# Optimization experiments

Measured on AMD Instinct MI355X. Metric: run time of the kernel, lower is better.

The kernel has to match this reference:

```python
import jax, jax.numpy as jnp
import numpy as np

N = 100000
EPS = 1e-5
NEG_SLOPE = 0.2


def gat_conv(x, src, dst, W, a_src, a_dst, b):
    # x: [N, din]; W: [dout, din]; a_src/a_dst/b: [dout]
    h = x @ W.T                              # [N, dout]
    alpha_s = h @ a_src                      # [N]
    alpha_d = h @ a_dst                      # [N]
    e = jax.nn.leaky_relu(alpha_s[src] + alpha_d[dst], NEG_SLOPE)  # [E]
    # segment softmax over incoming edges of each destination node
    emax = jax.ops.segment_max(e, dst, num_segments=N)
    ex = jnp.exp(e - emax[dst])
    denom = jax.ops.segment_sum(ex, dst, num_segments=N)
    alpha = ex / denom[dst]                  # [E]
    out = jax.ops.segment_sum(alpha[:, None] * h[src], dst, num_segments=N)
    return out + b


def batch_norm(x, gamma, beta):
    mu = jnp.mean(x, axis=0)
    var = jnp.var(x, axis=0)
    return gamma * (x - mu) * jax.lax.rsqrt(var + EPS) + beta


def setup_inputs() -> dict:
    key = jax.random.key(0)
    ks = jax.random.split(key, 20)
    din, dh, dout = 128, 128, 128
    E = 1600000
    x = jax.random.normal(ks[0], (N, din), dtype=jnp.float32)
    edge_index = jax.random.randint(ks[1], (2, E), 0, N, dtype=jnp.int32)
    def glorot(k, shape):
        fan = sum(shape)
        s = jnp.sqrt(6.0 / fan)
        return jax.random.uniform(k, shape, dtype=jnp.float32, minval=-s, maxval=s)
    inp = {"x": x, "edge_index": edge_index}
    dims = [(din, dh), (dh, dh), (dh, dout)]
    for l, (di, do) in enumerate(dims):
        inp[f"W{l}"] = glorot(ks[2 + 4 * l], (do, di))
        inp[f"a_src{l}"] = glorot(ks[3 + 4 * l], (do,)) * 0.1
        inp[f"a_dst{l}"] = glorot(ks[4 + 4 * l], (do,)) * 0.1
        inp[f"b{l}"] = jnp.zeros((do,), dtype=jnp.float32)
    for l in range(2):
        inp[f"gamma{l}"] = jnp.ones((dh,), dtype=jnp.float32)
        inp[f"beta{l}"] = jnp.zeros((dh,), dtype=jnp.float32)
    return inp


def reference(x, edge_index, W0, a_src0, a_dst0, b0, W1, a_src1, a_dst1, b1,
              W2, a_src2, a_dst2, b2, gamma0, beta0, gamma1, beta1):
    # add self-loops (PyG GATConv default)
    ar = jnp.arange(N, dtype=edge_index.dtype)
    src = jnp.concatenate([edge_index[0], ar])
    dst = jnp.concatenate([edge_index[1], ar])
    h = gat_conv(x, src, dst, W0, a_src0, a_dst0, b0)
    h = jax.nn.relu(batch_norm(h, gamma0, beta0))
    h = gat_conv(h, src, dst, W1, a_src1, a_dst1, b1)
    h = jax.nn.relu(batch_norm(h, gamma1, beta1))
    out = gat_conv(h, src, dst, W2, a_src2, a_dst2, b2)
    return out
```

## Files before the change

kernel.cpp:

```cpp
#include <hip/hip_runtime.h>
#include <cstdint>
#include <cstddef>

#define NN 100000
#define NP 100096
#define EE 1600000
#define ET 1700000
#define NBKT 196
#define TILE 2048
#define STAT_BLOCKS 400

typedef short  bf16x8 __attribute__((ext_vector_type(8)));
typedef float  f32x4  __attribute__((ext_vector_type(4)));

__device__ __forceinline__ unsigned short f2bf(float f) {
    unsigned int x = __builtin_bit_cast(unsigned int, f);
    x += 0x7FFFu + ((x >> 16) & 1u);
    return (unsigned short)(x >> 16);
}
__device__ __forceinline__ unsigned int pk2(float lo, float hi) {
    return ((unsigned int)f2bf(hi) << 16) | (unsigned int)f2bf(lo);
}
__device__ __forceinline__ float bflo(unsigned int u) {
    return __builtin_bit_cast(float, u << 16);
}
__device__ __forceinline__ float bfhi(unsigned int u) {
    return __builtin_bit_cast(float, u & 0xFFFF0000u);
}
__device__ __forceinline__ int unperm(int j) { return ((j & 7) << 4) | (j >> 3); }

__global__ void k_pre(const int* __restrict__ ei,
                      const float* __restrict__ W0, const float* __restrict__ W1,
                      const float* __restrict__ W2, unsigned short* __restrict__ Wb,
                      int* __restrict__ btot)
{
    const int t = threadIdx.x;
    const int b = blockIdx.x;
    if (b < 256) {
        __shared__ int h[256];
        h[t] = 0;
        __syncthreads();
        for (int e = b * 256 + t; e < ET; e += 256 * 256) {
            int d = (e < EE) ? ei[EE + e] : (e - EE);
            atomicAdd(&h[d >> 9], 1);
        }
        __syncthreads();
        if (h[t]) atomicAdd(&btot[t], h[t]);
    } else {
        int i = (b - 256) * 256 + t;
        int layer = i >> 14;
        const float* W = (layer == 0) ? W0 : (layer == 1) ? W1 : W2;
        int o  = i & 16383;
        int f  = o >> 3, e = o & 7;
        int nt = f >> 8, k0 = (f >> 6) & 3, lane = f & 63;
        int c  = lane & 15, q = lane >> 4;
        int k  = k0 * 32 + q * 8 + e;
        int col = (layer == 0) ? k : unperm(k);
        Wb[i] = f2bf(W[(nt * 16 + c) * 128 + col]);
    }
}

__global__ void k_bscan(const int* __restrict__ btot, int* __restrict__ bstart,
                        int* __restrict__ bcur, int* __restrict__ off) {
    __shared__ int s[256];
    int t = threadIdx.x;
    int v = (t < NBKT) ? btot[t] : 0;
    s[t] = v;
    __syncthreads();
    for (int o = 1; o < 256; o <<= 1) {
        int a = (t >= o) ? s[t - o] : 0;
        __syncthreads();
        s[t] += a;
        __syncthreads();
    }
    int ex = s[t] - v;
    if (t <= NBKT) bstart[t] = (t < NBKT) ? ex : ET;
    if (t == NBKT - 1) bstart[NBKT] = s[t];
    bcur[t] = ex;
    if (t == 0) off[NN] = ET;
}

__global__ __launch_bounds__(256) void k_bucket(
    const int* __restrict__ ei, int* __restrict__ bcur, unsigned int* __restrict__ bucketed)
{
    __shared__ int h4[4][256], woff[4][256], loff[256], gbase[256], sc[256];
    __shared__ unsigned int stage[TILE];
    __shared__ int gaddr[TILE];
    __shared__ int stot_s;
    const int t = threadIdx.x;
    const int w = t >> 6;
    const int e0 = blockIdx.x * TILE;

    h4[0][t] = 0; h4[1][t] = 0; h4[2][t] = 0; h4[3][t] = 0;
    __syncthreads();

    unsigned int pk[TILE / 256];
    int bk[TILE / 256];
#pragma unroll
    for (int i = 0; i < TILE / 256; ++i) {
        int e = e0 + i * 256 + t;
        bk[i] = -1;
        if (e < ET) {
            int s, d;
            if (e < EE) { s = ei[e]; d = ei[EE + e]; } else { s = e - EE; d = s; }
            bk[i] = d >> 9;
            pk[i] = ((unsigned int)(d & 511) << 17) | (unsigned int)s;
            atomicAdd(&h4[w][bk[i]], 1);
        }
    }
    __syncthreads();

    int h0 = h4[0][t], h1 = h4[1][t], h2 = h4[2][t], h3 = h4[3][t];
    int tot = h0 + h1 + h2 + h3;
    sc[t] = tot;
    __syncthreads();
    for (int o = 1; o < 256; o <<= 1) {
        int a = (t >= o) ? sc[t - o] : 0;
        __syncthreads();
        sc[t] += a;
        __syncthreads();
    }
    int lo = sc[t] - tot;
    loff[t] = lo;
    woff[0][t] = lo;
    woff[1][t] = lo + h0;
    woff[2][t] = lo + h0 + h1;
    woff[3][t] = lo + h0 + h1 + h2;
    if (t < NBKT && tot) gbase[t] = atomicAdd(&bcur[t], tot);
    if (t == 255) stot_s = sc[255];
    h4[0][t] = 0; h4[1][t] = 0; h4[2][t] = 0; h4[3][t] = 0;
    __syncthreads();

#pragma unroll
    for (int i = 0; i < TILE / 256; ++i) {
        if (bk[i] >= 0) {
            int b = bk[i];
            int r = woff[w][b] + atomicAdd(&h4[w][b], 1);
            stage[r] = pk[i];
            gaddr[r] = gbase[b] + (r - loff[b]);
        }
    }
    __syncthreads();

    const int stot = stot_s;
    for (int j = t; j < stot; j += 256)
        bucketed[gaddr[j]] = stage[j];
}

__global__ __launch_bounds__(256) void k_csr(
    const unsigned int* __restrict__ bucketed, const int* __restrict__ bstart,
    int* __restrict__ off, int* __restrict__ srcs)
{
    __shared__ int h[512], sc2[512], c2[512], sp[256];
    const int t = threadIdx.x;
    const int b = blockIdx.x;
    const int beg = bstart[b], end = bstart[b + 1];
    const int cnt = end - beg;

    h[t] = 0; h[t + 256] = 0; c2[t] = 0; c2[t + 256] = 0;
    __syncthreads();
    for (int i = t; i < cnt; i += 256)
        atomicAdd(&h[bucketed[beg + i] >> 17], 1);
    __syncthreads();

    int a0 = h[2 * t], a1 = h[2 * t + 1];
    sp[t] = a0 + a1;
    __syncthreads();
    for (int o = 1; o < 256; o <<= 1) {
        int a = (t >= o) ? sp[t - o] : 0;
        __syncthreads();
        sp[t] += a;
        __syncthreads();
    }
    int ep = sp[t] - (a0 + a1);
    sc2[2 * t] = ep;
    sc2[2 * t + 1] = ep + a0;
    __syncthreads();

    const int d0 = b << 9;
#pragma unroll
    for (int k = t; k < 512; k += 256) {
        int d = d0 + k;
        if (d < NN) off[d] = beg + sc2[k];
    }

    for (int i = t; i < cnt; i += 256) {
        unsigned int v = bucketed[beg + i];
        int ld = v >> 17;
        int r = atomicAdd(&c2[ld], 1);
        srcs[beg + sc2[ld] + r] = (int)(v & 0x1FFFFu);
    }
}

template<int MODE>
__global__ __launch_bounds__(256) void k_mfma(
    const void* __restrict__ Xv, const unsigned short* __restrict__ Wb,
    const float* __restrict__ gsum, const float* __restrict__ gsq,
    const float* __restrict__ gamma, const float* __restrict__ beta,
    const float* __restrict__ asrc, const float* __restrict__ adst,
    unsigned short* __restrict__ Hb, float* __restrict__ AS, float* __restrict__ AD)
{
    __shared__ float scale_s[128], shift_s[128];
    const int t    = threadIdx.x;
    const int lane = t & 63;
    const int c    = lane & 15;
    const int q    = lane >> 4;
    const int r0   = blockIdx.x * 64 + (t >> 6) * 16;
    const int row  = r0 + c;

    if (MODE) {
        if (t < 128) {
            int ot = unperm(t);
            float mu  = gsum[t] * (1.f / NN);
            float var = gsq[t] * (1.f / NN) - mu * mu;
            float sc  = gamma[ot] * rsqrtf(var + 1e-5f);
            scale_s[t] = sc;
            shift_s[t] = beta[ot] - mu * sc;
        }
        __syncthreads();
    }

    union { uint4 u; bf16x8 v; } Af[4];
    if (row < NN) {
        if (MODE) {
            const unsigned short* xp = (const unsigned short*)Xv + ((size_t)row << 7) + (q << 3);
#pragma unroll
            for (int k0 = 0; k0 < 4; ++k0) {
                uint4 r = *(const uint4*)(xp + (k0 << 5));
                const int kb = (k0 << 5) + (q << 3);
                float a0 = bflo(r.x), a1 = bfhi(r.x), a2 = bflo(r.y), a3 = bfhi(r.y);
                float a4 = bflo(r.z), a5 = bfhi(r.z), a6 = bflo(r.w), a7 = bfhi(r.w);
                float4 sA = *(const float4*)&scale_s[kb];
                float4 sB = *(const float4*)&scale_s[kb + 4];
                float4 hA = *(const float4*)&shift_s[kb];
                float4 hB = *(const float4*)&shift_s[kb + 4];
                a0 = fmaxf(0.f, fmaf(a0, sA.x, hA.x));
                a1 = fmaxf(0.f, fmaf(a1, sA.y, hA.y));
                a2 = fmaxf(0.f, fmaf(a2, sA.z, hA.z));
                a3 = fmaxf(0.f, fmaf(a3, sA.w, hA.w));
                a4 = fmaxf(0.f, fmaf(a4, sB.x, hB.x));
                a5 = fmaxf(0.f, fmaf(a5, sB.y, hB.y));
                a6 = fmaxf(0.f, fmaf(a6, sB.z, hB.z));
                a7 = fmaxf(0.f, fmaf(a7, sB.w, hB.w));
                Af[k0].u.x = pk2(a0, a1);
                Af[k0].u.y = pk2(a2, a3);
                Af[k0].u.z = pk2(a4, a5);
                Af[k0].u.w = pk2(a6, a7);
            }
        } else {
            const float* xp = (const float*)Xv + ((size_t)row << 7) + (q << 3);
#pragma unroll
            for (int k0 = 0; k0 < 4; ++k0) {
                float4 a = *(const float4*)(xp + (k0 << 5));
                float4 b = *(const float4*)(xp + (k0 << 5) + 4);
                Af[k0].u.x = pk2(a.x, a.y);
                Af[k0].u.y = pk2(a.z, a.w);
                Af[k0].u.z = pk2(b.x, b.y);
                Af[k0].u.w = pk2(b.z, b.w);
            }
        }
    } else {
#pragma unroll
        for (int k0 = 0; k0 < 4; ++k0) Af[k0].u = make_uint4(0, 0, 0, 0);
    }

    f32x4 acc[8];
#pragma unroll
    for (int nt = 0; nt < 8; ++nt) acc[nt] = (f32x4){0.f, 0.f, 0.f, 0.f};

#pragma unroll
    for (int nt = 0; nt < 8; ++nt) {
        union { uint4 u; bf16x8 v; } Bf[4];
#pragma unroll
        for (int k0 = 0; k0 < 4; ++k0)
            Bf[k0].u = *(const uint4*)(Wb + ((size_t)(((nt << 2) + k0) * 64 + lane) << 3));
#pragma unroll
        for (int k0 = 0; k0 < 4; ++k0)
            acc[nt] = __builtin_amdgcn_mfma_f32_16x16x32_bf16(Af[k0].v, Bf[k0].v, acc[nt], 0, 0, 0);
    }

    float ps[4] = {0.f, 0.f, 0.f, 0.f}, pd[4] = {0.f, 0.f, 0.f, 0.f};
#pragma unroll
    for (int nt = 0; nt < 8; ++nt) {
        float av = asrc[nt * 16 + c];
        float dv = adst[nt * 16 + c];
#pragma unroll
        for (int r = 0; r < 4; ++r) {
            ps[r] = fmaf(acc[nt][r], av, ps[r]);
            pd[r] = fmaf(acc[nt][r], dv, pd[r]);
        }
    }
#pragma unroll
    for (int m = 1; m < 16; m <<= 1) {
#pragma unroll
        for (int r = 0; r < 4; ++r) { ps[r] += __shfl_xor(ps[r], m); pd[r] += __shfl_xor(pd[r], m); }
    }
    if (c == 0) {
#pragma unroll
        for (int r = 0; r < 4; ++r) {
            int grow = r0 + q * 4 + r;
            if (grow < NN) { AS[grow] = ps[r]; AD[grow] = pd[r]; }
        }
    }

#pragma unroll
    for (int r = 0; r < 4; ++r) {
        int grow = r0 + q * 4 + r;
        if (grow < NN) {
            uint4 o;
            o.x = pk2(acc[0][r], acc[1][r]);
            o.y = pk2(acc[2][r], acc[3][r]);
            o.z = pk2(acc[4][r], acc[5][r]);
            o.w = pk2(acc[6][r], acc[7][r]);
            *(uint4*)(Hb + ((size_t)grow << 7) + (c << 3)) = o;
        }
    }
}

template<int OUTBF>
__global__ __launch_bounds__(256) void k_agg(
    const int* __restrict__ off, const int* __restrict__ srcs,
    const unsigned short* __restrict__ Hb, const float* __restrict__ AS,
    const float* __restrict__ AD, const float* __restrict__ bias,
    void* __restrict__ OUT)
{
    __shared__ uint2 s_e[4][64];
    const int wid  = threadIdx.x >> 6;
    const int lane = threadIdx.x & 63;
    const int g    = lane >> 4;
    const int x16  = lane & 15;
    const int n    = blockIdx.x * 4 + wid;
    const int beg = off[n], end = off[n + 1];
    const float adn = AD[n];

    float acc[8];
#pragma unroll
    for (int i = 0; i < 8; ++i) acc[i] = 0.f;
    float den = 0.f;

    for (int base = beg; base < end; base += 64) {
        int cnt = end - base; if (cnt > 64) cnt = 64;
        float wgt = 0.f; int s = 0;
        if (lane < cnt) {
            s = srcs[base + lane];
            float e = AS[s] + adn;
            e = (e > 0.f) ? e : 0.2f * e;
            wgt = __expf(e);
        }
        s_e[wid][lane] = make_uint2((unsigned int)s, __builtin_bit_cast(unsigned int, wgt));
        den += wgt;
        int rounds = (cnt + 3) >> 2;
        for (int j = 0; j < rounds; ++j) {
            uint2 ew = s_e[wid][(j << 2) + g];
            float wq = __builtin_bit_cast(float, ew.y);
            uint4 u = *((const uint4*)(Hb + ((size_t)ew.x << 7)) + x16);
            acc[0] = fmaf(wq, bflo(u.x), acc[0]);
            acc[1] = fmaf(wq, bfhi(u.x), acc[1]);
            acc[2] = fmaf(wq, bflo(u.y), acc[2]);
            acc[3] = fmaf(wq, bfhi(u.y), acc[3]);
            acc[4] = fmaf(wq, bflo(u.z), acc[4]);
            acc[5] = fmaf(wq, bfhi(u.z), acc[5]);
            acc[6] = fmaf(wq, bflo(u.w), acc[6]);
            acc[7] = fmaf(wq, bfhi(u.w), acc[7]);
        }
    }

#pragma unroll
    for (int i = 0; i < 8; ++i) {
        acc[i] += __shfl_xor(acc[i], 16);
        acc[i] += __shfl_xor(acc[i], 32);
    }
#pragma unroll
    for (int o = 32; o; o >>= 1) den += __shfl_xor(den, o);
    float inv = 1.f / den;

    if (g == 0) {
        float o8[8];
#pragma unroll
        for (int i = 0; i < 8; ++i)
            o8[i] = fmaf(acc[i], inv, bias[i * 16 + x16]);
        if (OUTBF) {
            uint4 pkd;
            pkd.x = pk2(o8[0], o8[1]); pkd.y = pk2(o8[2], o8[3]);
            pkd.z = pk2(o8[4], o8[5]); pkd.w = pk2(o8[6], o8[7]);
            *(uint4*)((unsigned short*)OUT + ((size_t)n << 7) + (x16 << 3)) = pkd;
        } else {
            float* op = (float*)OUT + ((size_t)n << 7) + x16;
#pragma unroll
            for (int i = 0; i < 8; ++i)
                op[i * 16] = o8[i];
        }
    }
}

__global__ __launch_bounds__(256) void k_colsum(const unsigned int* __restrict__ Xb,
                                                float* __restrict__ gsum, float* __restrict__ gsq) {
    __shared__ float ls[4][128], lq[4][128];
    const int t = threadIdx.x;
    const int c2 = t & 63;
    const int half = t >> 6;
    float s0 = 0.f, s1 = 0.f, q0 = 0.f, q1 = 0.f;
    for (int r = blockIdx.x * 4 + half; r < NN; r += STAT_BLOCKS * 4) {
        unsigned int v = Xb[(size_t)r * 64 + c2];
        float f0 = bflo(v), f1 = bfhi(v);
        s0 += f0; q0 += f0 * f0;
        s1 += f1; q1 += f1 * f1;
    }
    ls[half][2 * c2] = s0; ls[half][2 * c2 + 1] = s1;
    lq[half][2 * c2] = q0; lq[half][2 * c2 + 1] = q1;
    __syncthreads();
    if (t < 128) {
        float ss = ls[0][t] + ls[1][t] + ls[2][t] + ls[3][t];
        float qq = lq[0][t] + lq[1][t] + lq[2][t] + lq[3][t];
        atomicAdd(&gsum[t], ss);
        atomicAdd(&gsq[t], qq);
    }
}

extern "C" void kernel_launch(void* const* d_in, const int* in_sizes, int n_in,
                              void* d_out, int out_size, void* d_ws, size_t ws_size,
                              hipStream_t stream)
{
    const float* x  = (const float*)d_in[0];
    const int*   ei = (const int*)d_in[1];
    const float* Wm[3]  = {(const float*)d_in[2], (const float*)d_in[6],  (const float*)d_in[10]};
    const float* Asr[3] = {(const float*)d_in[3], (const float*)d_in[7],  (const float*)d_in[11]};
    const float* Ads[3] = {(const float*)d_in[4], (const float*)d_in[8],  (const float*)d_in[12]};
    const float* Bs[3]  = {(const float*)d_in[5], (const float*)d_in[9],  (const float*)d_in[13]};
    const float* gam[2] = {(const float*)d_in[14], (const float*)d_in[16]};
    const float* bet[2] = {(const float*)d_in[15], (const float*)d_in[17]};

    char* p = (char*)d_ws;
    auto carve = [&](size_t bytes) -> char* {
        char* r = p;
        p += (bytes + 255) & ~(size_t)255;
        return r;
    };
    int*   off_   = (int*)carve((size_t)(NN + 1) * 4);
    int*   srcs   = (int*)carve((size_t)ET * 4);
    unsigned int* bucketed = (unsigned int*)carve((size_t)ET * 4);
    int*   btot   = (int*)carve(256 * 4);
    float* gstat  = (float*)carve(4 * 128 * 4);
    int*   bstart = (int*)carve(260 * 4);
    int*   bcur   = (int*)carve(256 * 4);
    unsigned short* Hb  = (unsigned short*)carve((size_t)NP * 128 * 2);
    unsigned short* Wb  = (unsigned short*)carve((size_t)3 * 16384 * 2);
    float* AS    = (float*)carve((size_t)NN * 4);
    float* AD    = (float*)carve((size_t)NN * 4);

    float*          OUTf = (float*)d_out;
    unsigned short* OUTb = (unsigned short*)d_out;

    (void)hipMemsetAsync(btot, 0, 256 * 4 + 4 * 128 * 4, stream);

    k_pre<<<448, 256, 0, stream>>>(ei, Wm[0], Wm[1], Wm[2], Wb, btot);
    k_bscan<<<1, 256, 0, stream>>>(btot, bstart, bcur, off_);
    k_bucket<<<(ET + TILE - 1) / TILE, 256, 0, stream>>>(ei, bcur, bucketed);
    k_csr<<<NBKT, 256, 0, stream>>>(bucketed, bstart, off_, srcs);

    const int MFMA_GRID = NP / 64;

    k_mfma<0><<<MFMA_GRID, 256, 0, stream>>>(x, Wb, nullptr, nullptr, nullptr, nullptr,
                                             Asr[0], Ads[0], Hb, AS, AD);
    k_agg<1><<<NN / 4, 256, 0, stream>>>(off_, srcs, Hb, AS, AD, Bs[0], OUTb);
    k_colsum<<<STAT_BLOCKS, 256, 0, stream>>>((const unsigned int*)OUTb, gstat, gstat + 128);

    k_mfma<1><<<MFMA_GRID, 256, 0, stream>>>(OUTb, Wb + 16384, gstat, gstat + 128,
                                             gam[0], bet[0], Asr[1], Ads[1], Hb, AS, AD);
    k_agg<1><<<NN / 4, 256, 0, stream>>>(off_, srcs, Hb, AS, AD, Bs[1], OUTb);
    k_colsum<<<STAT_BLOCKS, 256, 0, stream>>>((const unsigned int*)OUTb, gstat + 256, gstat + 384);

    k_mfma<1><<<MFMA_GRID, 256, 0, stream>>>(OUTb, Wb + 32768, gstat + 256, gstat + 384,
                                             gam[1], bet[1], Asr[2], Ads[2], Hb, AS, AD);
    k_agg<0><<<NN / 4, 256, 0, stream>>>(off_, srcs, Hb, AS, AD, Bs[2], OUTf);
}
```

Measured before the change: 488.9 us.

## Precompute W^T·a attention vectors and fold bucket scan into consumers

Attention logits are now computed as x·(Wᵀa_src) and x·(Wᵀa_dst) directly from the input row during the A-fragment load, using vectors precomputed by an extra block in k_pre. This replaces the post-MFMA reduction over accumulator tiles with its cross-lane shuffles. Separately, the single-block k_bscan launch is removed and each k_bucket/k_csr block redoes the bucket prefix scan locally, which saves one launch but adds redundant scan work per block. Logits now come from fp32 inputs rather than the bf16-rounded matmul output, which slightly changes numerics.

```diff
diff --git a/kernel.cpp b/kernel.cpp
--- a/kernel.cpp
+++ b/kernel.cpp
@@ -28,11 +28,16 @@
     return __builtin_bit_cast(float, u & 0xFFFF0000u);
 }
 __device__ __forceinline__ int unperm(int j) { return ((j & 7) << 4) | (j >> 3); }
+__device__ __forceinline__ int permf(int c)  { return ((c & 15) << 3) | (c >> 4); }
 
 __global__ void k_pre(const int* __restrict__ ei,
                       const float* __restrict__ W0, const float* __restrict__ W1,
-                      const float* __restrict__ W2, unsigned short* __restrict__ Wb,
-                      int* __restrict__ btot)
+                      const float* __restrict__ W2,
+                      const float* __restrict__ as0, const float* __restrict__ ad0,
+                      const float* __restrict__ as1, const float* __restrict__ ad1,
+                      const float* __restrict__ as2, const float* __restrict__ ad2,
+                      unsigned short* __restrict__ Wb, int* __restrict__ btot,
+                      float* __restrict__ asv)
 {
     const int t = threadIdx.x;
     const int b = blockIdx.x;
@@ -46,7 +51,7 @@
         }
         __syncthreads();
         if (h[t]) atomicAdd(&btot[t], h[t]);
-    } else {
+    } else if (b < 448) {
         int i = (b - 256) * 256 + t;
         int layer = i >> 14;
         const float* W = (layer == 0) ? W0 : (layer == 1) ? W1 : W2;
@@ -57,33 +62,26 @@
         int k  = k0 * 32 + q * 8 + e;
         int col = (layer == 0) ? k : unperm(k);
         Wb[i] = f2bf(W[(nt * 16 + c) * 128 + col]);
-    }
-}
-
-__global__ void k_bscan(const int* __restrict__ btot, int* __restrict__ bstart,
-                        int* __restrict__ bcur, int* __restrict__ off) {
-    __shared__ int s[256];
-    int t = threadIdx.x;
-    int v = (t < NBKT) ? btot[t] : 0;
-    s[t] = v;
-    __syncthreads();
-    for (int o = 1; o < 256; o <<= 1) {
-        int a = (t >= o) ? s[t - o] : 0;
-        __syncthreads();
-        s[t] += a;
-        __syncthreads();
-    }
-    int ex = s[t] - v;
-    if (t <= NBKT) bstart[t] = (t < NBKT) ? ex : ET;
-    if (t == NBKT - 1) bstart[NBKT] = s[t];
-    bcur[t] = ex;
-    if (t == 0) off[NN] = ET;
+    } else {
+        const float* Wl[3] = {W0, W1, W2};
+        const float* Al[6] = {as0, ad0, as1, ad1, as2, ad2};
+        int vec = t >> 7, col = t & 127;
+        for (int l = 0; l < 3; ++l) {
+            const float* W = Wl[l];
+            const float* a = Al[2 * l + vec];
+            float s = 0.f;
+            for (int n = 0; n < 128; ++n) s += W[n * 128 + col] * a[n];
+            int dc = (l == 0) ? col : permf(col);
+            asv[l * 256 + vec * 128 + dc] = s;
+        }
+    }
 }
 
 __global__ __launch_bounds__(256) void k_bucket(
-    const int* __restrict__ ei, int* __restrict__ bcur, unsigned int* __restrict__ bucketed)
+    const int* __restrict__ ei, const int* __restrict__ btot,
+    int* __restrict__ bcur0, unsigned int* __restrict__ bucketed)
 {
-    __shared__ int h4[4][256], woff[4][256], loff[256], gbase[256], sc[256];
+    __shared__ int h4[4][256], woff[4][256], loff[256], gbase[256], sc[256], bst[256];
     __shared__ unsigned int stage[TILE];
     __shared__ int gaddr[TILE];
     __shared__ int stot_s;
@@ -91,8 +89,17 @@
     const int w = t >> 6;
     const int e0 = blockIdx.x * TILE;
 
+    const int v0 = btot[t];
+    bst[t] = v0;
     h4[0][t] = 0; h4[1][t] = 0; h4[2][t] = 0; h4[3][t] = 0;
     __syncthreads();
+    for (int o = 1; o < 256; o <<= 1) {
+        int a = (t >= o) ? bst[t - o] : 0;
+        __syncthreads();
+        bst[t] += a;
+        __syncthreads();
+    }
+    const int bstart_t = bst[t] - v0;
 
     unsigned int pk[TILE / 256];
     int bk[TILE / 256];
@@ -126,7 +133,7 @@
     woff[1][t] = lo + h0;
     woff[2][t] = lo + h0 + h1;
     woff[3][t] = lo + h0 + h1 + h2;
-    if (t < NBKT && tot) gbase[t] = atomicAdd(&bcur[t], tot);
+    if (t < NBKT && tot) gbase[t] = bstart_t + atomicAdd(&bcur0[t], tot);
     if (t == 255) stot_s = sc[255];
     h4[0][t] = 0; h4[1][t] = 0; h4[2][t] = 0; h4[3][t] = 0;
     __syncthreads();
@@ -148,17 +155,30 @@
 }
 
 __global__ __launch_bounds__(256) void k_csr(
-    const unsigned int* __restrict__ bucketed, const int* __restrict__ bstart,
+    const unsigned int* __restrict__ bucketed, const int* __restrict__ btot,
     int* __restrict__ off, int* __restrict__ srcs)
 {
-    __shared__ int h[512], sc2[512], c2[512], sp[256];
+    __shared__ int h[512], sc2[512], c2[512], sp[256], bst[256];
+    __shared__ int s_beg, s_end;
     const int t = threadIdx.x;
     const int b = blockIdx.x;
-    const int beg = bstart[b], end = bstart[b + 1];
+
+    const int v0 = btot[t];
+    bst[t] = v0;
+    __syncthreads();
+    for (int o = 1; o < 256; o <<= 1) {
+        int a = (t >= o) ? bst[t - o] : 0;
+        __syncthreads();
+        bst[t] += a;
+        __syncthreads();
+    }
+    if (t == b) { s_end = bst[b]; s_beg = bst[b] - v0; }
+    if (b == 0 && t == 0) off[NN] = ET;
+    h[t] = 0; h[t + 256] = 0; c2[t] = 0; c2[t + 256] = 0;
+    __syncthreads();
+    const int beg = s_beg, end = s_end;
     const int cnt = end - beg;
 
-    h[t] = 0; h[t + 256] = 0; c2[t] = 0; c2[t + 256] = 0;
-    __syncthreads();
     for (int i = t; i < cnt; i += 256)
         atomicAdd(&h[bucketed[beg + i] >> 17], 1);
     __syncthreads();
@@ -197,10 +217,10 @@
     const void* __restrict__ Xv, const unsigned short* __restrict__ Wb,
     const float* __restrict__ gsum, const float* __restrict__ gsq,
     const float* __restrict__ gamma, const float* __restrict__ beta,
-    const float* __restrict__ asrc, const float* __restrict__ adst,
+    const float* __restrict__ wsd,
     unsigned short* __restrict__ Hb, float* __restrict__ AS, float* __restrict__ AD)
 {
-    __shared__ float scale_s[128], shift_s[128];
+    __shared__ float ws_s[128], wd_s[128], scale_s[128], shift_s[128];
     const int t    = threadIdx.x;
     const int lane = t & 63;
     const int c    = lane & 15;
@@ -208,8 +228,10 @@
     const int r0   = blockIdx.x * 64 + (t >> 6) * 16;
     const int row  = r0 + c;
 
-    if (MODE) {
-        if (t < 128) {
+    if (t < 128) {
+        ws_s[t] = wsd[t];
+        wd_s[t] = wsd[128 + t];
+        if (MODE) {
             int ot = unperm(t);
             float mu  = gsum[t] * (1.f / NN);
             float var = gsq[t] * (1.f / NN) - mu * mu;
@@ -217,10 +239,11 @@
             scale_s[t] = sc;
             shift_s[t] = beta[ot] - mu * sc;
         }
-        __syncthreads();
-    }
+    }
+    __syncthreads();
 
     union { uint4 u; bf16x8 v; } Af[4];
+    float asp = 0.f, adp = 0.f;
     if (row < NN) {
         if (MODE) {
             const unsigned short* xp = (const unsigned short*)Xv + ((size_t)row << 7) + (q << 3);
@@ -242,6 +265,14 @@
                 a5 = fmaxf(0.f, fmaf(a5, sB.y, hB.y));
                 a6 = fmaxf(0.f, fmaf(a6, sB.z, hB.z));
                 a7 = fmaxf(0.f, fmaf(a7, sB.w, hB.w));
+                float4 wa = *(const float4*)&ws_s[kb];
+                float4 wb = *(const float4*)&ws_s[kb + 4];
+                float4 da = *(const float4*)&wd_s[kb];
+                float4 db = *(const float4*)&wd_s[kb + 4];
+                asp = fmaf(a0, wa.x, fmaf(a1, wa.y, fmaf(a2, wa.z, fmaf(a3, wa.w, asp))));
+                asp = fmaf(a4, wb.x, fmaf(a5, wb.y, fmaf(a6, wb.z, fmaf(a7, wb.w, asp))));
+                adp = fmaf(a0, da.x, fmaf(a1, da.y, fmaf(a2, da.z, fmaf(a3, da.w, adp))));
+                adp = fmaf(a4, db.x, fmaf(a5, db.y, fmaf(a6, db.z, fmaf(a7, db.w, adp))));
                 Af[k0].u.x = pk2(a0, a1);
                 Af[k0].u.y = pk2(a2, a3);
                 Af[k0].u.z = pk2(a4, a5);
@@ -253,6 +284,15 @@
             for (int k0 = 0; k0 < 4; ++k0) {
                 float4 a = *(const float4*)(xp + (k0 << 5));
                 float4 b = *(const float4*)(xp + (k0 << 5) + 4);
+                const int kb = (k0 << 5) + (q << 3);
+                float4 wa = *(const float4*)&ws_s[kb];
+                float4 wb = *(const float4*)&ws_s[kb + 4];
+                float4 da = *(const float4*)&wd_s[kb];
+                float4 db = *(const float4*)&wd_s[kb + 4];
+                asp = fmaf(a.x, wa.x, fmaf(a.y, wa.y, fmaf(a.z, wa.z, fmaf(a.w, wa.w, asp))));
+                asp = fmaf(b.x, wb.x, fmaf(b.y, wb.y, fmaf(b.z, wb.z, fmaf(b.w, wb.w, asp))));
+                adp = fmaf(a.x, da.x, fmaf(a.y, da.y, fmaf(a.z, da.z, fmaf(a.w, da.w, adp))));
+                adp = fmaf(b.x, db.x, fmaf(b.y, db.y, fmaf(b.z, db.z, fmaf(b.w, db.w, adp))));
                 Af[k0].u.x = pk2(a.x, a.y);
                 Af[k0].u.y = pk2(a.z, a.w);
                 Af[k0].u.z = pk2(b.x, b.y);
@@ -264,6 +304,13 @@
         for (int k0 = 0; k0 < 4; ++k0) Af[k0].u = make_uint4(0, 0, 0, 0);
     }
 
+    asp += __shfl_xor(asp, 16); asp += __shfl_xor(asp, 32);
+    adp += __shfl_xor(adp, 16); adp += __shfl_xor(adp, 32);
+    if (lane < 16) {
+        int grow = r0 + lane;
+        if (grow < NN) { AS[grow] = asp; AD[grow] = adp; }
+    }
+
     f32x4 acc[8];
 #pragma unroll
     for (int nt = 0; nt < 8; ++nt) acc[nt] = (f32x4){0.f, 0.f, 0.f, 0.f};
@@ -277,30 +324,6 @@
 #pragma unroll
         for (int k0 = 0; k0 < 4; ++k0)
             acc[nt] = __builtin_amdgcn_mfma_f32_16x16x32_bf16(Af[k0].v, Bf[k0].v, acc[nt], 0, 0, 0);
-    }
-
-    float ps[4] = {0.f, 0.f, 0.f, 0.f}, pd[4] = {0.f, 0.f, 0.f, 0.f};
-#pragma unroll
-    for (int nt = 0; nt < 8; ++nt) {
-        float av = asrc[nt * 16 + c];
-        float dv = adst[nt * 16 + c];
-#pragma unroll
-        for (int r = 0; r < 4; ++r) {
-            ps[r] = fmaf(acc[nt][r], av, ps[r]);
-            pd[r] = fmaf(acc[nt][r], dv, pd[r]);
-        }
-    }
-#pragma unroll
-    for (int m = 1; m < 16; m <<= 1) {
-#pragma unroll
-        for (int r = 0; r < 4; ++r) { ps[r] += __shfl_xor(ps[r], m); pd[r] += __shfl_xor(pd[r], m); }
-    }
-    if (c == 0) {
-#pragma unroll
-        for (int r = 0; r < 4; ++r) {
-            int grow = r0 + q * 4 + r;
-            if (grow < NN) { AS[grow] = ps[r]; AD[grow] = pd[r]; }
-        }
     }
 
 #pragma unroll
@@ -440,9 +463,9 @@
     int*   srcs   = (int*)carve((size_t)ET * 4);
     unsigned int* bucketed = (unsigned int*)carve((size_t)ET * 4);
     int*   btot   = (int*)carve(256 * 4);
+    int*   bcur0  = (int*)carve(256 * 4);
     float* gstat  = (float*)carve(4 * 128 * 4);
-    int*   bstart = (int*)carve(260 * 4);
-    int*   bcur   = (int*)carve(256 * 4);
+    float* asv    = (float*)carve(3 * 256 * 4);
     unsigned short* Hb  = (unsigned short*)carve((size_t)NP * 128 * 2);
     unsigned short* Wb  = (unsigned short*)carve((size_t)3 * 16384 * 2);
     float* AS    = (float*)carve((size_t)NN * 4);
@@ -451,26 +474,27 @@
     float*          OUTf = (float*)d_out;
     unsigned short* OUTb = (unsigned short*)d_out;
 
-    (void)hipMemsetAsync(btot, 0, 256 * 4 + 4 * 128 * 4, stream);
-
-    k_pre<<<448, 256, 0, stream>>>(ei, Wm[0], Wm[1], Wm[2], Wb, btot);
-    k_bscan<<<1, 256, 0, stream>>>(btot, bstart, bcur, off_);
-    k_bucket<<<(ET + TILE - 1) / TILE, 256, 0, stream>>>(ei, bcur, bucketed);
-    k_csr<<<NBKT, 256, 0, stream>>>(bucketed, bstart, off_, srcs);
+    (void)hipMemsetAsync(btot, 0, 256 * 4 + 256 * 4 + 4 * 128 * 4, stream);
+
+    k_pre<<<449, 256, 0, stream>>>(ei, Wm[0], Wm[1], Wm[2],
+                                   Asr[0], Ads[0], Asr[1], Ads[1], Asr[2], Ads[2],
+                                   Wb, btot, asv);
+    k_bucket<<<(ET + TILE - 1) / TILE, 256, 0, stream>>>(ei, btot, bcur0, bucketed);
+    k_csr<<<NBKT, 256, 0, stream>>>(bucketed, btot, off_, srcs);
 
     const int MFMA_GRID = NP / 64;
 
     k_mfma<0><<<MFMA_GRID, 256, 0, stream>>>(x, Wb, nullptr, nullptr, nullptr, nullptr,
-                                             Asr[0], Ads[0], Hb, AS, AD);
+                                             asv, Hb, AS, AD);
     k_agg<1><<<NN / 4, 256, 0, stream>>>(off_, srcs, Hb, AS, AD, Bs[0], OUTb);
     k_colsum<<<STAT_BLOCKS, 256, 0, stream>>>((const unsigned int*)OUTb, gstat, gstat + 128);
 
     k_mfma<1><<<MFMA_GRID, 256, 0, stream>>>(OUTb, Wb + 16384, gstat, gstat + 128,
-                                             gam[0], bet[0], Asr[1], Ads[1], Hb, AS, AD);
+                                             gam[0], bet[0], asv + 256, Hb, AS, AD);
     k_agg<1><<<NN / 4, 256, 0, stream>>>(off_, srcs, Hb, AS, AD, Bs[1], OUTb);
     k_colsum<<<STAT_BLOCKS, 256, 0, stream>>>((const unsigned int*)OUTb, gstat + 256, gstat + 384);
 
     k_mfma<1><<<MFMA_GRID, 256, 0, stream>>>(OUTb, Wb + 32768, gstat + 256, gstat + 384,
-                                             gam[1], bet[1], Asr[2], Ads[2], Hb, AS, AD);
+                                             gam[1], bet[1], asv + 512, Hb, AS, AD);
     k_agg<0><<<NN / 4, 256, 0, stream>>>(off_, srcs, Hb, AS, AD, Bs[2], OUTf);
 }
```

Result: no change. 487.1 us (-0.4%).
